# Performance work log

Measured on AMD Instinct MI355X. Metric: run time of the kernel, lower is better.

Reference implementation:

```python
import jax, jax.numpy as jnp
import numpy as np

D_MODEL = 2048
N_HEADS = 16
HEAD_DIM = D_MODEL // N_HEADS
MLP_DIM = 4 * D_MODEL
RMS_EPS = 1e-6
MASK_VALUE = -1e9  # fp32 path in the original


def setup_inputs() -> dict:
    key = jax.random.key(0)
    ks = jax.random.split(key, 8)
    B, S = 2, 2048
    scale = 0.02
    return {
        "x": jax.random.normal(ks[0], (B, S, D_MODEL), dtype=jnp.float32),
        "attention_mask": jnp.ones((B, S), dtype=jnp.int32),
        "w_norm_attn": jnp.ones((D_MODEL,), dtype=jnp.float32),
        "wq": jax.random.normal(ks[1], (D_MODEL, D_MODEL), dtype=jnp.float32) * scale,
        "wk": jax.random.normal(ks[2], (D_MODEL, D_MODEL), dtype=jnp.float32) * scale,
        "wv": jax.random.normal(ks[3], (D_MODEL, D_MODEL), dtype=jnp.float32) * scale,
        "wo": jax.random.normal(ks[4], (D_MODEL, D_MODEL), dtype=jnp.float32) * scale,
        "w_norm_mlp": jnp.ones((D_MODEL,), dtype=jnp.float32),
        "w_up": jax.random.normal(ks[5], (MLP_DIM, D_MODEL), dtype=jnp.float32) * scale,
        "w_down": jax.random.normal(ks[6], (D_MODEL, MLP_DIM), dtype=jnp.float32) * scale,
    }


def _rmsnorm(x, w, eps=RMS_EPS):
    rms = jax.lax.rsqrt(jnp.mean(x * x, axis=-1, keepdims=True) + eps)
    return x * rms * w


def _split_heads(x):  # [B,S,D] -> [B,H,S,Dh]
    B, S, _ = x.shape
    return x.reshape(B, S, N_HEADS, HEAD_DIM).transpose(0, 2, 1, 3)


def reference(x, attention_mask, w_norm_attn, wq, wk, wv, wo, w_norm_mlp, w_up, w_down):
    B, S, _ = x.shape
    residual = x
    h = _rmsnorm(x, w_norm_attn)
    # nn.Linear(no bias): y = h @ W.T
    q = _split_heads(h @ wq.T)  # [B,H,S,Dh]
    k = _split_heads(h @ wk.T)
    v = _split_heads(h @ wv.T)

    scale = 1.0 / np.sqrt(HEAD_DIM)
    scores = jnp.einsum("bhqd,bhkd->bhqk", q, k) * scale  # [B,H,S,S]

    q_pos = jnp.arange(S)[:, None]
    k_pos = jnp.arange(S)[None, :]
    causal = k_pos <= q_pos  # [S,S]
    scores = jnp.where(causal[None, None], scores, MASK_VALUE)

    key_mask = attention_mask.astype(bool)  # [B,S]
    scores = jnp.where(key_mask[:, None, None, :], scores, MASK_VALUE)

    probs = jax.nn.softmax(scores.astype(jnp.float32), axis=-1).astype(q.dtype)
    probs = jnp.nan_to_num(probs, nan=0.0, posinf=0.0, neginf=0.0)

    att = jnp.einsum("bhqk,bhkd->bhqd", probs, v)  # [B,H,S,Dh]
    att = att.transpose(0, 2, 1, 3).reshape(B, S, D_MODEL)
    x = residual + att @ wo.T

    residual = x
    h = _rmsnorm(x, w_norm_mlp)
    h = jax.nn.gelu(h @ w_up.T, approximate=False)  # F.gelu default is exact erf
    x = residual + h @ w_down.T
    return x
```

## Files before the change

kernel.cpp:

```cpp
#include <hip/hip_runtime.h>

typedef unsigned short u16;
typedef __bf16 bf16x8 __attribute__((ext_vector_type(8)));
typedef float f32x4 __attribute__((ext_vector_type(4)));

#define SEQ 2048
#define DM 2048
#define NH 16
#define DHD 128
#define MLPD 8192
#define ATT_SCALE 0.08838834764831845f

__device__ __forceinline__ float bf2f(u16 u) {
  union { unsigned int i; float f; } c; c.i = ((unsigned int)u) << 16; return c.f;
}
__device__ __forceinline__ u16 f2bf(float f) {
  union { float f; unsigned int i; } c; c.f = f;
  unsigned int u = c.i;
  u += 0x7FFFu + ((u >> 16) & 1u);
  return (u16)(u >> 16);
}

__device__ __forceinline__ bool path_is_bf16(const unsigned* chk) {
  return chk[0] == 0x3F803F80u;
}

__device__ __forceinline__ void gl_lds16(const void* g, void* l) {
  __builtin_amdgcn_global_load_lds(
      (const __attribute__((address_space(1))) void*)g,
      (__attribute__((address_space(3))) void*)l, 16, 0, 0);
}

template <typename TIN>
__global__ __launch_bounds__(256) void rms_x(const TIN* __restrict__ in,
                                             const TIN* __restrict__ wn,
                                             u16* __restrict__ out,
                                             const unsigned* __restrict__ chk,
                                             unsigned want) {
  if ((path_is_bf16(chk) ? 1u : 0u) != want) return;
  const int row = blockIdx.x;
  const int t = threadIdx.x;
  float f[8], wv[8];
  if constexpr (sizeof(TIN) == 4) {
    const float* p = (const float*)in + (size_t)row * DM + t * 8;
    float4 a = *(const float4*)p, b = *(const float4*)(p + 4);
    f[0]=a.x; f[1]=a.y; f[2]=a.z; f[3]=a.w; f[4]=b.x; f[5]=b.y; f[6]=b.z; f[7]=b.w;
    const float* wp = (const float*)wn + t * 8;
    float4 c = *(const float4*)wp, d = *(const float4*)(wp + 4);
    wv[0]=c.x; wv[1]=c.y; wv[2]=c.z; wv[3]=c.w; wv[4]=d.x; wv[5]=d.y; wv[6]=d.z; wv[7]=d.w;
  } else {
    union { uint4 u; u16 s[8]; } v;
    v.u = *(const uint4*)((const u16*)in + (size_t)row * DM + t * 8);
    union { uint4 u; u16 s[8]; } wu;
    wu.u = *(const uint4*)((const u16*)wn + t * 8);
#pragma unroll
    for (int i = 0; i < 8; i++) { f[i] = bf2f(v.s[i]); wv[i] = bf2f(wu.s[i]); }
  }
  float ss = 0.f;
#pragma unroll
  for (int i = 0; i < 8; i++) ss += f[i] * f[i];
#pragma unroll
  for (int off = 32; off >= 1; off >>= 1) ss += __shfl_xor(ss, off, 64);
  __shared__ float ws4[4];
  if ((t & 63) == 0) ws4[t >> 6] = ss;
  __syncthreads();
  float tot = ws4[0] + ws4[1] + ws4[2] + ws4[3];
  float rms = rsqrtf(tot * (1.0f / DM) + 1e-6f);
  union { uint4 u; u16 s[8]; } o;
#pragma unroll
  for (int i = 0; i < 8; i++) o.s[i] = f2bf(f[i] * rms * wv[i]);
  *(uint4*)(out + (size_t)row * DM + t * 8) = o.u;
}

template <int EPI, typename TB, typename TC>
__global__ __launch_bounds__(256, 2) void gemm_x(const u16* __restrict__ A,
                                                 const TB* __restrict__ B,
                                                 TC* __restrict__ C,
                                                 const TC* __restrict__ res,
                                                 int N, int K,
                                                 int Ald, int Bld, int Cld,
                                                 const unsigned* __restrict__ chk,
                                                 unsigned want) {
  if ((path_is_bf16(chk) ? 1u : 0u) != want) return;
  __shared__ u16 lA[128 * 32];
  __shared__ u16 lB[128 * 32];
  const int t = threadIdx.x;
  const int lane = t & 63;
  const int w = t >> 6;
  const int x = lane & 15;
  const int qd = lane >> 4;
  const int wr = w >> 1, wc = w & 1;
  const int m0 = blockIdx.y * 128, n0 = blockIdx.x * 128;

  const int c0 = t, c1 = t + 256;
  const u16* gA0 = A + (size_t)(m0 + (c0 >> 2)) * Ald + (c0 & 3) * 8;
  const u16* gA1 = A + (size_t)(m0 + (c1 >> 2)) * Ald + (c1 & 3) * 8;
  const TB* gB0 = B + (size_t)(n0 + (c0 >> 2)) * Bld + (c0 & 3) * 8;
  const TB* gB1 = B + (size_t)(n0 + (c1 >> 2)) * Bld + (c1 & 3) * 8;
  u16* sA0 = lA + c0 * 8; u16* sA1 = lA + c1 * 8;
  u16* sB0 = lB + c0 * 8; u16* sB1 = lB + c1 * 8;

  const u16* aAddr[4]; const u16* bAddr[4];
#pragma unroll
  for (int i = 0; i < 4; i++) {
    aAddr[i] = lA + (wr * 64 + i * 16 + x) * 32 + qd * 8;
    bAddr[i] = lB + (wc * 64 + i * 16 + x) * 32 + qd * 8;
  }

  const f32x4 ZV = {0.f, 0.f, 0.f, 0.f};
  f32x4 acc[4][4];
#pragma unroll
  for (int i = 0; i < 4; i++)
#pragma unroll
    for (int j = 0; j < 4; j++) acc[i][j] = ZV;

  for (int kk = 0; kk < K; kk += 32) {
    gl_lds16(gA0, sA0); gl_lds16(gA1, sA1);
    if constexpr (sizeof(TB) == 2) {
      gl_lds16(gB0, sB0); gl_lds16(gB1, sB1);
    } else {
      float4 a0 = *(const float4*)gB0, a1 = *(const float4*)(gB0 + 4);
      float4 b0 = *(const float4*)gB1, b1 = *(const float4*)(gB1 + 4);
      union { uint4 u; u16 s[8]; } p0, p1;
      p0.s[0]=f2bf(a0.x); p0.s[1]=f2bf(a0.y); p0.s[2]=f2bf(a0.z); p0.s[3]=f2bf(a0.w);
      p0.s[4]=f2bf(a1.x); p0.s[5]=f2bf(a1.y); p0.s[6]=f2bf(a1.z); p0.s[7]=f2bf(a1.w);
      p1.s[0]=f2bf(b0.x); p1.s[1]=f2bf(b0.y); p1.s[2]=f2bf(b0.z); p1.s[3]=f2bf(b0.w);
      p1.s[4]=f2bf(b1.x); p1.s[5]=f2bf(b1.y); p1.s[6]=f2bf(b1.z); p1.s[7]=f2bf(b1.w);
      *(uint4*)sB0 = p0.u;
      *(uint4*)sB1 = p1.u;
    }
    gA0 += 32; gA1 += 32; gB0 += 32; gB1 += 32;
    __syncthreads();
    bf16x8 aF[4], bF[4];
#pragma unroll
    for (int i = 0; i < 4; i++) {
      aF[i] = *(const bf16x8*)aAddr[i];
      bF[i] = *(const bf16x8*)bAddr[i];
    }
#pragma unroll
    for (int i = 0; i < 4; i++)
#pragma unroll
      for (int j = 0; j < 4; j++)
        acc[i][j] = __builtin_amdgcn_mfma_f32_16x16x32_bf16(aF[i], bF[j], acc[i][j], 0, 0, 0);
    __syncthreads();
  }

#pragma unroll
  for (int i = 0; i < 4; i++) {
    const int rg = m0 + wr * 64 + i * 16 + qd * 4;
#pragma unroll
    for (int j = 0; j < 4; j++) {
      const int cg = n0 + wc * 64 + j * 16 + x;
#pragma unroll
      for (int r = 0; r < 4; r++) {
        float v = acc[i][j][r];
        size_t idx = (size_t)(rg + r) * Cld + cg;
        if (EPI == 1) {
          if constexpr (sizeof(TC) == 4) v += ((const float*)res)[idx];
          else v += bf2f(((const u16*)res)[idx]);
        } else if (EPI == 2) {
          v = 0.5f * v * (1.0f + erff(v * 0.70710678118654752f));
        }
        if constexpr (sizeof(TC) == 4) ((float*)C)[idx] = v;
        else ((u16*)C)[idx] = f2bf(v);
      }
    }
  }
}

__global__ __launch_bounds__(256, 2) void attn_kernel(const u16* __restrict__ Q,
                                                      const u16* __restrict__ Kb,
                                                      const u16* __restrict__ V,
                                                      const int* __restrict__ mask,
                                                      u16* __restrict__ O) {
  __shared__ u16 lK[64 * 136];
  __shared__ u16 lV[128 * 72];
  __shared__ u16 lP[4 * 32 * 72];
  __shared__ float lBias[64];

  const int t = threadIdx.x;
  const int lane = t & 63;
  const int w = t >> 6;
  const int x = lane & 15;
  const int qd = lane >> 4;
  const int qt = blockIdx.x;
  const int b = blockIdx.y >> 4;
  const int h = blockIdx.y & 15;
  const int q0 = qt * 128 + w * 32;
  const size_t batchRow = (size_t)b * SEQ;

  bf16x8 qF[2][4];
#pragma unroll
  for (int mt = 0; mt < 2; mt++)
#pragma unroll
    for (int kf = 0; kf < 4; kf++)
      qF[mt][kf] = *(const bf16x8*)(Q + (batchRow + q0 + mt * 16 + x) * DM +
                                    h * DHD + kf * 32 + qd * 8);

  const f32x4 ZV = {0.f, 0.f, 0.f, 0.f};
  f32x4 oAcc[2][8];
#pragma unroll
  for (int mt = 0; mt < 2; mt++)
#pragma unroll
    for (int dt = 0; dt < 8; dt++) oAcc[mt][dt] = ZV;
  float mrow[2][4], lrow[2][4];
#pragma unroll
  for (int mt = 0; mt < 2; mt++)
#pragma unroll
    for (int r = 0; r < 4; r++) { mrow[mt][r] = -1e30f; lrow[mt][r] = 0.f; }

  const int nkt = min(SEQ / 64, 2 * qt + 2);
  u16* lPw = lP + w * (32 * 72);

  for (int kt = 0; kt < nkt; kt++) {
    const int k0 = kt * 64;
#pragma unroll
    for (int ii = 0; ii < 4; ii++) {
      int c = ii * 256 + t;
      int kr = c >> 4, ko = (c & 15) * 8;
      uint4 kvv = *(const uint4*)(Kb + (batchRow + k0 + kr) * DM + h * DHD + ko);
      *(uint4*)(lK + kr * 136 + ko) = kvv;
      union { uint4 u; u16 s[8]; } vv;
      vv.u = *(const uint4*)(V + (batchRow + k0 + kr) * DM + h * DHD + ko);
#pragma unroll
      for (int i = 0; i < 8; i++) lV[(ko + i) * 72 + kr] = vv.s[i];
    }
    if (t < 64) lBias[t] = mask[b * SEQ + k0 + t] ? 0.f : -1e9f;
    __syncthreads();

    f32x4 sAcc[2][4];
#pragma unroll
    for (int mt = 0; mt < 2; mt++)
#pragma unroll
      for (int nt = 0; nt < 4; nt++) sAcc[mt][nt] = ZV;
#pragma unroll
    for (int nt = 0; nt < 4; nt++) {
      bf16x8 kB[4];
#pragma unroll
      for (int kf = 0; kf < 4; kf++)
        kB[kf] = *(const bf16x8*)(lK + (nt * 16 + x) * 136 + kf * 32 + qd * 8);
#pragma unroll
      for (int mt = 0; mt < 2; mt++)
#pragma unroll
        for (int kf = 0; kf < 4; kf++)
          sAcc[mt][nt] = __builtin_amdgcn_mfma_f32_16x16x32_bf16(qF[mt][kf], kB[kf], sAcc[mt][nt], 0, 0, 0);
    }

#pragma unroll
    for (int mt = 0; mt < 2; mt++) {
#pragma unroll
      for (int r = 0; r < 4; r++) {
        const int qg = q0 + mt * 16 + qd * 4 + r;
        float sv[4]; float mx = -1e30f;
#pragma unroll
        for (int nt = 0; nt < 4; nt++) {
          int kg = k0 + nt * 16 + x;
          float s = sAcc[mt][nt][r] * ATT_SCALE + lBias[nt * 16 + x];
          if (kg > qg) s = -1e9f;
          sv[nt] = s;
          mx = fmaxf(mx, s);
        }
#pragma unroll
        for (int off = 1; off < 16; off <<= 1) mx = fmaxf(mx, __shfl_xor(mx, off, 16));
        const float mnew = fmaxf(mrow[mt][r], mx);
        const float alpha = __expf(mrow[mt][r] - mnew);
        mrow[mt][r] = mnew;
        float rs = 0.f;
#pragma unroll
        for (int nt = 0; nt < 4; nt++) {
          float p = __expf(sv[nt] - mnew);
          rs += p;
          lPw[(mt * 16 + qd * 4 + r) * 72 + nt * 16 + x] = f2bf(p);
        }
#pragma unroll
        for (int off = 1; off < 16; off <<= 1) rs += __shfl_xor(rs, off, 16);
        lrow[mt][r] = lrow[mt][r] * alpha + rs;
#pragma unroll
        for (int dt = 0; dt < 8; dt++) oAcc[mt][dt][r] *= alpha;
      }
    }
    __syncthreads();

#pragma unroll
    for (int kf2 = 0; kf2 < 2; kf2++) {
      bf16x8 aP[2];
#pragma unroll
      for (int mt = 0; mt < 2; mt++)
        aP[mt] = *(const bf16x8*)(lPw + (mt * 16 + x) * 72 + kf2 * 32 + qd * 8);
#pragma unroll
      for (int dt = 0; dt < 8; dt++) {
        bf16x8 vB = *(const bf16x8*)(lV + (dt * 16 + x) * 72 + kf2 * 32 + qd * 8);
#pragma unroll
        for (int mt = 0; mt < 2; mt++)
          oAcc[mt][dt] = __builtin_amdgcn_mfma_f32_16x16x32_bf16(aP[mt], vB, oAcc[mt][dt], 0, 0, 0);
      }
    }
    __syncthreads();
  }

#pragma unroll
  for (int mt = 0; mt < 2; mt++) {
    float inv[4];
#pragma unroll
    for (int r = 0; r < 4; r++) inv[r] = 1.f / lrow[mt][r];
#pragma unroll
    for (int dt = 0; dt < 8; dt++)
#pragma unroll
      for (int r = 0; r < 4; r++) {
        const int qg = q0 + mt * 16 + qd * 4 + r;
        O[(batchRow + qg) * DM + h * DHD + dt * 16 + x] = f2bf(oAcc[mt][dt][r] * inv[r]);
      }
  }
}

extern "C" void kernel_launch(void* const* d_in, const int* in_sizes, int n_in,
                              void* d_out, int out_size, void* d_ws, size_t ws_size,
                              hipStream_t stream) {
  (void)in_sizes; (void)n_in; (void)out_size; (void)ws_size;
  const int* mask = (const int*)d_in[1];
  const unsigned* chk = (const unsigned*)d_in[2];
  u16* ws = (u16*)d_ws;

  const size_t SZ = (size_t)4096 * DM;
  u16* hn  = ws + 0 * SZ;
  u16* q   = ws + 1 * SZ;
  u16* k   = ws + 2 * SZ;
  u16* v   = ws + 3 * SZ;
  u16* att = hn;
  u16* h2  = q;
  u16* g   = k;

  const int M = 4096;
  const int MH = 4096;
  dim3 g2k(DM / 128, M / 128), gmh(MH / 128, M / 128);

  {
    const float* x   = (const float*)d_in[0];
    const float* wna = (const float*)d_in[2];
    const float* wq  = (const float*)d_in[3];
    const float* wk  = (const float*)d_in[4];
    const float* wv  = (const float*)d_in[5];
    const float* wo  = (const float*)d_in[6];
    const float* wnm = (const float*)d_in[7];
    const float* wup = (const float*)d_in[8];
    const float* wdn = (const float*)d_in[9];
    float* out = (float*)d_out;
    rms_x<float><<<M, 256, 0, stream>>>(x, wna, hn, chk, 0);
    gemm_x<0, float, u16><<<g2k, 256, 0, stream>>>(hn, wq, q, (u16*)nullptr, DM, DM, DM, DM, DM, chk, 0);
    gemm_x<0, float, u16><<<g2k, 256, 0, stream>>>(hn, wk, k, (u16*)nullptr, DM, DM, DM, DM, DM, chk, 0);
    gemm_x<0, float, u16><<<g2k, 256, 0, stream>>>(hn, wv, v, (u16*)nullptr, DM, DM, DM, DM, DM, chk, 0);
  }
  {
    const u16* x   = (const u16*)d_in[0];
    const u16* wna = (const u16*)d_in[2];
    const u16* wq  = (const u16*)d_in[3];
    const u16* wk  = (const u16*)d_in[4];
    const u16* wv  = (const u16*)d_in[5];
    rms_x<u16><<<M, 256, 0, stream>>>(x, wna, hn, chk, 1);
    gemm_x<0, u16, u16><<<g2k, 256, 0, stream>>>(hn, wq, q, (u16*)nullptr, DM, DM, DM, DM, DM, chk, 1);
    gemm_x<0, u16, u16><<<g2k, 256, 0, stream>>>(hn, wk, k, (u16*)nullptr, DM, DM, DM, DM, DM, chk, 1);
    gemm_x<0, u16, u16><<<g2k, 256, 0, stream>>>(hn, wv, v, (u16*)nullptr, DM, DM, DM, DM, DM, chk, 1);
  }

  attn_kernel<<<dim3(SEQ / 128, 32), 256, 0, stream>>>(q, k, v, mask, att);

  {
    const float* x   = (const float*)d_in[0];
    const float* wo  = (const float*)d_in[6];
    const float* wnm = (const float*)d_in[7];
    const float* wup = (const float*)d_in[8];
    const float* wdn = (const float*)d_in[9];
    float* out = (float*)d_out;
    gemm_x<1, float, float><<<g2k, 256, 0, stream>>>(att, wo, out, x, DM, DM, DM, DM, DM, chk, 0);
    rms_x<float><<<M, 256, 0, stream>>>(out, wnm, h2, chk, 0);
    gemm_x<2, float, u16><<<gmh, 256, 0, stream>>>(h2, wup, g, (u16*)nullptr, MH, DM, DM, DM, MH, chk, 0);
    gemm_x<1, float, float><<<g2k, 256, 0, stream>>>(g, wdn, out, out, DM, MH, MH, MLPD, DM, chk, 0);
    gemm_x<2, float, u16><<<gmh, 256, 0, stream>>>(h2, wup + (size_t)MH * DM, g, (u16*)nullptr, MH, DM, DM, DM, MH, chk, 0);
    gemm_x<1, float, float><<<g2k, 256, 0, stream>>>(g, wdn + MH, out, out, DM, MH, MH, MLPD, DM, chk, 0);
  }
  {
    const u16* x   = (const u16*)d_in[0];
    const u16* wo  = (const u16*)d_in[6];
    const u16* wnm = (const u16*)d_in[7];
    const u16* wup = (const u16*)d_in[8];
    const u16* wdn = (const u16*)d_in[9];
    u16* out = (u16*)d_out;
    gemm_x<1, u16, u16><<<g2k, 256, 0, stream>>>(att, wo, out, x, DM, DM, DM, DM, DM, chk, 1);
    rms_x<u16><<<M, 256, 0, stream>>>(out, wnm, h2, chk, 1);
    gemm_x<2, u16, u16><<<gmh, 256, 0, stream>>>(h2, wup, g, (u16*)nullptr, MH, DM, DM, DM, MH, chk, 1);
    gemm_x<1, u16, u16><<<g2k, 256, 0, stream>>>(g, wdn, out, out, DM, MH, MH, MLPD, DM, chk, 1);
    gemm_x<2, u16, u16><<<gmh, 256, 0, stream>>>(h2, wup + (size_t)MH * DM, g, (u16*)nullptr, MH, DM, DM, DM, MH, chk, 1);
    gemm_x<1, u16, u16><<<g2k, 256, 0, stream>>>(g, wdn + MH, out, out, DM, MH, MH, MLPD, DM, chk, 1);
  }
}
```

Measured before the change: 1.327 ms.

## Pre-transpose V, use direct global-to-LDS swizzled loads and lazy softmax rescale in attention

A separate kernel now transposes V into a per-head [D, S] layout, so the attention kernel can fill LDS for K and V with direct 16-byte global-to-LDS copies into XOR-swizzled unpadded tiles. This replaces the scalar transposing stores. The attention kernel also drops a barrier between the P write and the PV matmul, since each wave only reads its own P slice. It skips the online-softmax rescale unless the row max grows by more than 8, and reorders q-tiles so heavy and light causal blocks alternate. Launch bounds allow 3 blocks per CU. The cost is an extra transpose pass over V and some workspace aliasing changes.

```diff
diff --git a/kernel.cpp b/kernel.cpp
--- a/kernel.cpp
+++ b/kernel.cpp
@@ -168,14 +168,44 @@
   }
 }
 
-__global__ __launch_bounds__(256, 2) void attn_kernel(const u16* __restrict__ Q,
+#define VT_PAD 130
+__global__ __launch_bounds__(256) void vtrans(const u16* __restrict__ v,
+                                              u16* __restrict__ vt) {
+  __shared__ __align__(16) u16 tile[128 * VT_PAD];
+  const int st = blockIdx.x;
+  const int bh = blockIdx.y;
+  const int b = bh >> 4, h = bh & 15;
+  const int t = threadIdx.x;
+#pragma unroll
+  for (int i = 0; i < 8; i++) {
+    int c = i * 256 + t;
+    int s = c >> 4, d8 = (c & 15) * 8;
+    union { uint4 u; u16 e[8]; } x;
+    x.u = *(const uint4*)(v + ((size_t)(b * SEQ + st * 128 + s)) * DM + h * DHD + d8);
+#pragma unroll
+    for (int j = 0; j < 8; j++) tile[(d8 + j) * VT_PAD + s] = x.e[j];
+  }
+  __syncthreads();
+#pragma unroll
+  for (int i = 0; i < 8; i++) {
+    int c = i * 256 + t;
+    int d = c >> 4, s8 = (c & 15) * 8;
+    const u16* src = tile + d * VT_PAD + s8;
+    union { uint4 u; unsigned wd[4]; } o;
+#pragma unroll
+    for (int j = 0; j < 4; j++) o.wd[j] = *(const unsigned*)(src + j * 2);
+    *(uint4*)(vt + ((size_t)(bh * DHD + d)) * SEQ + st * 128 + s8) = o.u;
+  }
+}
+
+__global__ __launch_bounds__(256, 3) void attn_kernel(const u16* __restrict__ Q,
                                                       const u16* __restrict__ Kb,
-                                                      const u16* __restrict__ V,
+                                                      const u16* __restrict__ Vt,
                                                       const int* __restrict__ mask,
                                                       u16* __restrict__ O) {
-  __shared__ u16 lK[64 * 136];
-  __shared__ u16 lV[128 * 72];
-  __shared__ u16 lP[4 * 32 * 72];
+  __shared__ __align__(16) u16 lK[64 * 128];
+  __shared__ __align__(16) u16 lV[128 * 64];
+  __shared__ __align__(16) u16 lP[4 * 32 * 64];
   __shared__ float lBias[64];
 
   const int t = threadIdx.x;
@@ -183,11 +213,13 @@
   const int w = t >> 6;
   const int x = lane & 15;
   const int qd = lane >> 4;
-  const int qt = blockIdx.x;
+  const int jj = blockIdx.x;
+  const int qt = (jj & 1) ? (jj >> 1) : (15 - (jj >> 1));
   const int b = blockIdx.y >> 4;
   const int h = blockIdx.y & 15;
   const int q0 = qt * 128 + w * 32;
   const size_t batchRow = (size_t)b * SEQ;
+  const size_t vtBase = (size_t)blockIdx.y * DHD * SEQ;
 
   bf16x8 qF[2][4];
 #pragma unroll
@@ -210,20 +242,21 @@
     for (int r = 0; r < 4; r++) { mrow[mt][r] = -1e30f; lrow[mt][r] = 0.f; }
 
   const int nkt = min(SEQ / 64, 2 * qt + 2);
-  u16* lPw = lP + w * (32 * 72);
+  u16* lPw = lP + w * (32 * 64);
 
   for (int kt = 0; kt < nkt; kt++) {
     const int k0 = kt * 64;
 #pragma unroll
     for (int ii = 0; ii < 4; ii++) {
       int c = ii * 256 + t;
-      int kr = c >> 4, ko = (c & 15) * 8;
-      uint4 kvv = *(const uint4*)(Kb + (batchRow + k0 + kr) * DM + h * DHD + ko);
-      *(uint4*)(lK + kr * 136 + ko) = kvv;
-      union { uint4 u; u16 s[8]; } vv;
-      vv.u = *(const uint4*)(V + (batchRow + k0 + kr) * DM + h * DHD + ko);
-#pragma unroll
-      for (int i = 0; i < 8; i++) lV[(ko + i) * 72 + kr] = vv.s[i];
+      int kr = c >> 4, lc = (c & 15) ^ (kr & 7);
+      gl_lds16(Kb + (batchRow + k0 + kr) * DM + h * DHD + lc * 8, lK + c * 8);
+    }
+#pragma unroll
+    for (int ii = 0; ii < 4; ii++) {
+      int c = ii * 256 + t;
+      int d = c >> 3, lc = (c & 7) ^ (d & 7);
+      gl_lds16(Vt + vtBase + (size_t)d * SEQ + k0 + lc * 8, lV + c * 8);
     }
     if (t < 64) lBias[t] = mask[b * SEQ + k0 + t] ? 0.f : -1e9f;
     __syncthreads();
@@ -235,10 +268,13 @@
       for (int nt = 0; nt < 4; nt++) sAcc[mt][nt] = ZV;
 #pragma unroll
     for (int nt = 0; nt < 4; nt++) {
+      const int n = nt * 16 + x;
       bf16x8 kB[4];
 #pragma unroll
-      for (int kf = 0; kf < 4; kf++)
-        kB[kf] = *(const bf16x8*)(lK + (nt * 16 + x) * 136 + kf * 32 + qd * 8);
+      for (int kf = 0; kf < 4; kf++) {
+        int pc = (kf * 4 + qd) ^ (n & 7);
+        kB[kf] = *(const bf16x8*)(lK + n * 128 + pc * 8);
+      }
 #pragma unroll
       for (int mt = 0; mt < 2; mt++)
 #pragma unroll
@@ -250,7 +286,8 @@
     for (int mt = 0; mt < 2; mt++) {
 #pragma unroll
       for (int r = 0; r < 4; r++) {
-        const int qg = q0 + mt * 16 + qd * 4 + r;
+        const int qrow = mt * 16 + qd * 4 + r;
+        const int qg = q0 + qrow;
         float sv[4]; float mx = -1e30f;
 #pragma unroll
         for (int nt = 0; nt < 4; nt++) {
@@ -262,34 +299,44 @@
         }
 #pragma unroll
         for (int off = 1; off < 16; off <<= 1) mx = fmaxf(mx, __shfl_xor(mx, off, 16));
-        const float mnew = fmaxf(mrow[mt][r], mx);
-        const float alpha = __expf(mrow[mt][r] - mnew);
-        mrow[mt][r] = mnew;
+        float mold = mrow[mt][r];
+        if (!__all(mx - mold <= 8.f)) {
+          const float mnew = fmaxf(mold, mx);
+          const float alpha = __expf(mold - mnew);
+          mrow[mt][r] = mnew;
+          lrow[mt][r] *= alpha;
+#pragma unroll
+          for (int dt = 0; dt < 8; dt++) oAcc[mt][dt][r] *= alpha;
+          mold = mnew;
+        }
         float rs = 0.f;
 #pragma unroll
         for (int nt = 0; nt < 4; nt++) {
-          float p = __expf(sv[nt] - mnew);
+          float p = __expf(sv[nt] - mold);
           rs += p;
-          lPw[(mt * 16 + qd * 4 + r) * 72 + nt * 16 + x] = f2bf(p);
+          const int col = nt * 16 + x;
+          lPw[qrow * 64 + (((col >> 3) ^ (qrow & 7)) * 8) + (col & 7)] = f2bf(p);
         }
 #pragma unroll
         for (int off = 1; off < 16; off <<= 1) rs += __shfl_xor(rs, off, 16);
-        lrow[mt][r] = lrow[mt][r] * alpha + rs;
-#pragma unroll
-        for (int dt = 0; dt < 8; dt++) oAcc[mt][dt][r] *= alpha;
-      }
-    }
-    __syncthreads();
+        lrow[mt][r] += rs;
+      }
+    }
 
 #pragma unroll
     for (int kf2 = 0; kf2 < 2; kf2++) {
       bf16x8 aP[2];
 #pragma unroll
-      for (int mt = 0; mt < 2; mt++)
-        aP[mt] = *(const bf16x8*)(lPw + (mt * 16 + x) * 72 + kf2 * 32 + qd * 8);
+      for (int mt = 0; mt < 2; mt++) {
+        const int m = mt * 16 + x;
+        int pc = (kf2 * 4 + qd) ^ (m & 7);
+        aP[mt] = *(const bf16x8*)(lPw + m * 64 + pc * 8);
+      }
 #pragma unroll
       for (int dt = 0; dt < 8; dt++) {
-        bf16x8 vB = *(const bf16x8*)(lV + (dt * 16 + x) * 72 + kf2 * 32 + qd * 8);
+        const int d = dt * 16 + x;
+        int pc = (kf2 * 4 + qd) ^ (d & 7);
+        bf16x8 vB = *(const bf16x8*)(lV + d * 64 + pc * 8);
 #pragma unroll
         for (int mt = 0; mt < 2; mt++)
           oAcc[mt][dt] = __builtin_amdgcn_mfma_f32_16x16x32_bf16(aP[mt], vB, oAcc[mt][dt], 0, 0, 0);
@@ -326,7 +373,8 @@
   u16* q   = ws + 1 * SZ;
   u16* k   = ws + 2 * SZ;
   u16* v   = ws + 3 * SZ;
-  u16* att = hn;
+  u16* vt  = hn;
+  u16* att = v;
   u16* h2  = q;
   u16* g   = k;
 
@@ -340,11 +388,6 @@
     const float* wq  = (const float*)d_in[3];
     const float* wk  = (const float*)d_in[4];
     const float* wv  = (const float*)d_in[5];
-    const float* wo  = (const float*)d_in[6];
-    const float* wnm = (const float*)d_in[7];
-    const float* wup = (const float*)d_in[8];
-    const float* wdn = (const float*)d_in[9];
-    float* out = (float*)d_out;
     rms_x<float><<<M, 256, 0, stream>>>(x, wna, hn, chk, 0);
     gemm_x<0, float, u16><<<g2k, 256, 0, stream>>>(hn, wq, q, (u16*)nullptr, DM, DM, DM, DM, DM, chk, 0);
     gemm_x<0, float, u16><<<g2k, 256, 0, stream>>>(hn, wk, k, (u16*)nullptr, DM, DM, DM, DM, DM, chk, 0);
@@ -362,7 +405,8 @@
     gemm_x<0, u16, u16><<<g2k, 256, 0, stream>>>(hn, wv, v, (u16*)nullptr, DM, DM, DM, DM, DM, chk, 1);
   }
 
-  attn_kernel<<<dim3(SEQ / 128, 32), 256, 0, stream>>>(q, k, v, mask, att);
+  vtrans<<<dim3(SEQ / 128, 32), 256, 0, stream>>>(v, vt);
+  attn_kernel<<<dim3(SEQ / 128, 32), 256, 0, stream>>>(q, k, vt, mask, att);
 
   {
     const float* x   = (const float*)d_in[0];
```

Measured after the change: 1.719 ms. +29.5%, slower.
